# Performance work log

Measured on AMD Instinct MI355X. Metric: run time of the kernel, lower is better.

The kernel has to match this reference:

```python
import jax, jax.numpy as jnp
import numpy as np

N = 50000          # nodes
E = 1600000        # edges (before self-loops)
IN = 512           # in_channels
H = 8              # heads
C1 = 8             # per-head channels of conv1 (== heads)
OUT = 64           # out_channels
SLOPE = 0.2        # GATConv leaky_relu negative slope


def setup_inputs() -> dict:
    key = jax.random.key(0)
    ks = jax.random.split(key, 10)
    x = jax.random.normal(ks[0], (N, IN), jnp.float32)
    edge_index = jax.random.randint(ks[1], (2, E), 0, N, dtype=jnp.int64)
    s1 = 1.0 / np.sqrt(IN)
    s2 = 1.0 / np.sqrt(H * C1)
    W1 = jax.random.normal(ks[2], (IN, H * C1), jnp.float32) * s1
    att_src1 = jax.random.normal(ks[3], (H, C1), jnp.float32) * s2
    att_dst1 = jax.random.normal(ks[4], (H, C1), jnp.float32) * s2
    b1 = jnp.zeros((H * C1,), jnp.float32)
    W2 = jax.random.normal(ks[5], (H * C1, OUT), jnp.float32) * s2
    att_src2 = jax.random.normal(ks[6], (1, OUT), jnp.float32) * 0.1
    att_dst2 = jax.random.normal(ks[7], (1, OUT), jnp.float32) * 0.1
    b2 = jnp.zeros((OUT,), jnp.float32)
    return {"x": x, "edge_index": edge_index, "W1": W1, "att_src1": att_src1,
            "att_dst1": att_dst1, "b1": b1, "W2": W2, "att_src2": att_src2,
            "att_dst2": att_dst2, "b2": b2}


def gat_layer(x, src, dst, W, a_src, a_dst, b, heads, ch, concat):
    n = x.shape[0]
    h = (x @ W).reshape(n, heads, ch)                       # [N,H,C]
    alpha_src = jnp.einsum('nhc,hc->nh', h, a_src)          # [N,H]
    alpha_dst = jnp.einsum('nhc,hc->nh', h, a_dst)
    e = jax.nn.leaky_relu(alpha_src[src] + alpha_dst[dst], SLOPE)  # [Etot,H]
    # segment softmax over incoming edges of each destination node
    m = jax.ops.segment_max(e, dst, num_segments=n)
    ex = jnp.exp(e - m[dst])
    denom = jax.ops.segment_sum(ex, dst, num_segments=n)
    alpha = ex / (denom[dst] + 1e-16)                       # [Etot,H]
    out = jax.ops.segment_sum(h[src] * alpha[:, :, None], dst, num_segments=n)
    out = out.reshape(n, heads * ch) if concat else out.mean(axis=1)
    return out + b


def reference(x, edge_index, W1, att_src1, att_dst1, b1, W2, att_src2, att_dst2, b2):
    n = x.shape[0]
    loops = jnp.arange(n, dtype=edge_index.dtype)           # add_self_loops=True
    src = jnp.concatenate([edge_index[0], loops])
    dst = jnp.concatenate([edge_index[1], loops])
    h = jax.nn.elu(gat_layer(x, src, dst, W1, att_src1, att_dst1, b1, H, C1, True))
    # F.dropout in eval mode is identity
    out = gat_layer(h, src, dst, W2, att_src2, att_dst2, b2, 1, OUT, False)
    return jax.nn.log_softmax(out, axis=-1)
```

## Files before the change

kernel.cpp:

```cpp
#include <hip/hip_runtime.h>
#include <hip/hip_bf16.h>
#include <math.h>


#define WAVE 64
#define NPB_SHIFT 7
#define NB_MAX 512
#define NBLK 128
#define CAP 6144

__device__ inline float wred_sum(float v) {
#pragma unroll
    for (int off = 32; off > 0; off >>= 1) v += __shfl_xor(v, off);
    return v;
}
__device__ inline float wred_max(float v) {
#pragma unroll
    for (int off = 32; off > 0; off >>= 1) v = fmaxf(v, __shfl_xor(v, off));
    return v;
}

__global__ __launch_bounds__(256) void bucket_count(const int* __restrict__ ei,
                                                    int* __restrict__ hist,
                                                    int E, int Et, int NB, int epb) {
    __shared__ int lh[NB_MAX];
    for (int t = threadIdx.x; t < NB; t += 256) lh[t] = 0;
    __syncthreads();
    int e0 = blockIdx.x * epb;
    int e1 = min(e0 + epb, Et);
    for (int e = e0 + threadIdx.x; e < e1; e += 256) {
        int d = (e < E) ? ei[E + e] : (e - E);
        atomicAdd(&lh[d >> NPB_SHIFT], 1);
    }
    __syncthreads();
    for (int t = threadIdx.x; t < NB; t += 256)
        hist[blockIdx.x * NB + t] = lh[t];
}

__global__ __launch_bounds__(512) void bucket_scan(int* __restrict__ hist,
                                                   int* __restrict__ bBase,
                                                   int* __restrict__ rowptr,
                                                   int NB, int nblk, int n) {
    __shared__ int tot[NB_MAX];
    for (int b = threadIdx.x; b < NB; b += 512) {
        int s = 0;
        for (int j = 0; j < nblk; ++j) s += hist[j * NB + b];
        tot[b] = s;
    }
    __syncthreads();
    if (threadIdx.x == 0) {
        int run = 0;
        for (int b = 0; b < NB; ++b) { int t = tot[b]; tot[b] = run; bBase[b] = run; run += t; }
        bBase[NB] = run;
        rowptr[n] = run;
    }
    __syncthreads();
    for (int b = threadIdx.x; b < NB; b += 512) {
        int run = tot[b];
        for (int j = 0; j < nblk; ++j) { int t = hist[j * NB + b]; hist[j * NB + b] = run; run += t; }
    }
}

__global__ __launch_bounds__(256) void bucket_scatter(const int* __restrict__ ei,
                                                      const int* __restrict__ hist,
                                                      unsigned* __restrict__ region,
                                                      int E, int Et, int NB, int epb) {
    __shared__ int gb[NB_MAX];
    __shared__ int off[NB_MAX];
    for (int t = threadIdx.x; t < NB; t += 256) { gb[t] = hist[blockIdx.x * NB + t]; off[t] = 0; }
    __syncthreads();
    int e0 = blockIdx.x * epb;
    int e1 = min(e0 + epb, Et);
    for (int e = e0 + threadIdx.x; e < e1; e += 256) {
        int s, d;
        if (e < E) { s = ei[e]; d = ei[E + e]; }
        else       { s = d = e - E; }
        int b = d >> NPB_SHIFT;
        int p = gb[b] + atomicAdd(&off[b], 1);
        region[p] = (unsigned)s | ((unsigned)(d & 127) << 16);
    }
}

__global__ __launch_bounds__(256) void bucket_build(unsigned* __restrict__ region,
                                                    const int* __restrict__ bBase,
                                                    int* __restrict__ rowptr, int n) {
    __shared__ int deg[128], rp[129], cur[128];
    __shared__ unsigned short sb[CAP];
    int b = blockIdx.x;
    int base = bBase[b];
    int cnt  = min(bBase[b + 1] - base, CAP);
    int tid  = threadIdx.x;
    if (tid < 128) { deg[tid] = 0; cur[tid] = 0; }
    __syncthreads();
    for (int i = tid; i < cnt; i += 256)
        atomicAdd(&deg[region[base + i] >> 16], 1);
    __syncthreads();
    if (tid == 0) {
        int run = 0;
        for (int t = 0; t < 128; ++t) { rp[t] = run; run += deg[t]; }
        rp[128] = run;
    }
    __syncthreads();
    int nodeLo = b << NPB_SHIFT;
    if (tid < 128 && nodeLo + tid < n) rowptr[nodeLo + tid] = base + rp[tid];
    for (int i = tid; i < cnt; i += 256) {
        unsigned v = region[base + i];
        int dl = v >> 16;
        int p = rp[dl] + atomicAdd(&cur[dl], 1);
        sb[p] = (unsigned short)(v & 0xFFFFu);
    }
    __syncthreads();
    for (int i = tid; i < cnt; i += 256)
        region[base + i] = (unsigned)sb[i];
}

__global__ __launch_bounds__(256) void gemm64(const float* __restrict__ X,
                                              const float* __restrict__ W,
                                              float* __restrict__ O, int nrows, int K) {
    __shared__ float xs[32][68];
    __shared__ float ws[32][68];
    int tid = threadIdx.x;
    int bm = blockIdx.x * 64;
    int tx = tid & 15;
    int ty = tid >> 4;
    float acc[4][4] = {{0.f}};
    for (int k0 = 0; k0 < K; k0 += 32) {
#pragma unroll
        for (int i = 0; i < 2; ++i) {
            int p = tid + i * 256;
            int row = p >> 3, k4 = p & 7;
            float4 v = {0.f, 0.f, 0.f, 0.f};
            if (bm + row < nrows)
                v = *(const float4*)(X + (size_t)(bm + row) * K + k0 + k4 * 4);
            xs[k4 * 4 + 0][row] = v.x; xs[k4 * 4 + 1][row] = v.y;
            xs[k4 * 4 + 2][row] = v.z; xs[k4 * 4 + 3][row] = v.w;
        }
#pragma unroll
        for (int i = 0; i < 2; ++i) {
            int p = tid + i * 256;
            int kr = p >> 4, c4 = p & 15;
            float4 v = *(const float4*)(W + (size_t)(k0 + kr) * 64 + c4 * 4);
            ws[kr][c4 * 4 + 0] = v.x; ws[kr][c4 * 4 + 1] = v.y;
            ws[kr][c4 * 4 + 2] = v.z; ws[kr][c4 * 4 + 3] = v.w;
        }
        __syncthreads();
#pragma unroll
        for (int kk = 0; kk < 32; ++kk) {
            float a[4], bq[4];
#pragma unroll
            for (int i = 0; i < 4; ++i) a[i] = xs[kk][ty * 4 + i];
#pragma unroll
            for (int j = 0; j < 4; ++j) bq[j] = ws[kk][tx * 4 + j];
#pragma unroll
            for (int i = 0; i < 4; ++i)
#pragma unroll
                for (int j = 0; j < 4; ++j) acc[i][j] = fmaf(a[i], bq[j], acc[i][j]);
        }
        __syncthreads();
    }
    int row0 = bm + ty * 4;
#pragma unroll
    for (int i = 0; i < 4; ++i) {
        int r = row0 + i;
        if (r < nrows) {
            float4 v = {acc[i][0], acc[i][1], acc[i][2], acc[i][3]};
            *(float4*)(O + (size_t)r * 64 + tx * 4) = v;
        }
    }
}

__global__ __launch_bounds__(256) void alpha1_kernel(const float* __restrict__ H1,
                                                     const float* __restrict__ as1,
                                                     const float* __restrict__ ad1,
                                                     float* __restrict__ asrc,
                                                     float* __restrict__ adst, int n) {
    int idx = blockIdx.x * 256 + threadIdx.x;
    if (idx >= n * 8) return;
    int h = idx & 7;
    const float* hp = H1 + (size_t)(idx >> 3) * 64 + h * 8;
    float s = 0.f, d = 0.f;
#pragma unroll
    for (int c = 0; c < 8; ++c) {
        float v = hp[c];
        s = fmaf(v, as1[h * 8 + c], s);
        d = fmaf(v, ad1[h * 8 + c], d);
    }
    asrc[idx] = s;
    adst[idx] = d;
}

__global__ __launch_bounds__(256) void alpha2_kernel(const float* __restrict__ H2,
                                                     const float* __restrict__ as2,
                                                     const float* __restrict__ ad2,
                                                     float* __restrict__ asrc,
                                                     float* __restrict__ adst, int n) {
    int node = blockIdx.x * 4 + (threadIdx.x >> 6);
    int lane = threadIdx.x & 63;
    if (node >= n) return;
    float v = H2[(size_t)node * 64 + lane];
    float s = wred_sum(v * as2[lane]);
    float d = wred_sum(v * ad2[lane]);
    if (lane == 0) { asrc[node] = s; adst[node] = d; }
}

__global__ __launch_bounds__(256) void agg1_kernel(const float* __restrict__ H1,
                                                   const float* __restrict__ asrc,
                                                   const float* __restrict__ adst,
                                                   const int* __restrict__ rowptr,
                                                   const int* __restrict__ csrc,
                                                   const float* __restrict__ b1,
                                                   float* __restrict__ out1, int n) {
    __shared__ float wbuf[4][64][8];
    __shared__ int   sbuf[4][64];
    int wid  = threadIdx.x >> 6;
    int lane = threadIdx.x & 63;
    int node = blockIdx.x * 4 + wid;
    if (node >= n) return;
    int h = lane >> 3;
    int beg = rowptr[node], end = rowptr[node + 1];

    float ad[8];
    *(float4*)&ad[0] = *(const float4*)&adst[(size_t)node * 8];
    *(float4*)&ad[4] = *(const float4*)&adst[(size_t)node * 8 + 4];

    float lsum[8];
#pragma unroll
    for (int i = 0; i < 8; ++i) lsum[i] = 0.f;
    float acc0 = 0.f, acc1 = 0.f;

    for (int c0 = beg; c0 < end; c0 += 64) {
        int e = c0 + lane;
        if (e < end) {
            int s = csrc[e];
            sbuf[wid][lane] = s;
            float a[8], p[8];
            *(float4*)&a[0] = *(const float4*)&asrc[(size_t)s * 8];
            *(float4*)&a[4] = *(const float4*)&asrc[(size_t)s * 8 + 4];
#pragma unroll
            for (int i = 0; i < 8; ++i) {
                float t = a[i] + ad[i];
                t = t > 0.f ? t : 0.2f * t;
                p[i] = __expf(t);
                lsum[i] += p[i];
            }
            *(float4*)&wbuf[wid][lane][0] = *(float4*)&p[0];
            *(float4*)&wbuf[wid][lane][4] = *(float4*)&p[4];
        }
        int cnt = min(64, end - c0);
        int i = 0;
        for (; i + 3 < cnt; i += 4) {
            int s0 = sbuf[wid][i + 0], s1 = sbuf[wid][i + 1];
            int s2 = sbuf[wid][i + 2], s3 = sbuf[wid][i + 3];
            float w0 = wbuf[wid][i + 0][h], w1 = wbuf[wid][i + 1][h];
            float w2 = wbuf[wid][i + 2][h], w3 = wbuf[wid][i + 3][h];
            float g0 = H1[(size_t)s0 * 64 + lane];
            float g1 = H1[(size_t)s1 * 64 + lane];
            float g2 = H1[(size_t)s2 * 64 + lane];
            float g3 = H1[(size_t)s3 * 64 + lane];
            acc0 = fmaf(g0, w0, acc0);
            acc1 = fmaf(g1, w1, acc1);
            acc0 = fmaf(g2, w2, acc0);
            acc1 = fmaf(g3, w3, acc1);
        }
        for (; i < cnt; ++i) {
            int s   = sbuf[wid][i];
            float w = wbuf[wid][i][h];
            acc0 = fmaf(H1[(size_t)s * 64 + lane], w, acc0);
        }
    }
    float acc = acc0 + acc1;
#pragma unroll
    for (int off = 32; off > 0; off >>= 1)
#pragma unroll
        for (int i = 0; i < 8; ++i) lsum[i] += __shfl_xor(lsum[i], off);
    float L = lsum[0];
#pragma unroll
    for (int i = 1; i < 8; ++i) if (h == i) L = lsum[i];
    float o = acc / (L + 1e-16f) + b1[lane];
    out1[(size_t)node * 64 + lane] = o > 0.f ? o : expm1f(o);
}

__global__ __launch_bounds__(256) void agg2_kernel(const float* __restrict__ H2,
                                                   const float* __restrict__ asrc,
                                                   const float* __restrict__ adst,
                                                   const int* __restrict__ rowptr,
                                                   const int* __restrict__ csrc,
                                                   const float* __restrict__ b2,
                                                   float* __restrict__ out, int n) {
    __shared__ float wbuf[4][64];
    __shared__ int   sbuf[4][64];
    int wid  = threadIdx.x >> 6;
    int lane = threadIdx.x & 63;
    int node = blockIdx.x * 4 + wid;
    if (node >= n) return;
    int beg = rowptr[node], end = rowptr[node + 1];
    float ad = adst[node];

    float lsum = 0.f, acc0 = 0.f, acc1 = 0.f;
    for (int c0 = beg; c0 < end; c0 += 64) {
        int e = c0 + lane;
        if (e < end) {
            int s = csrc[e];
            sbuf[wid][lane] = s;
            float t = asrc[s] + ad;
            t = t > 0.f ? t : 0.2f * t;
            float p = __expf(t);
            lsum += p;
            wbuf[wid][lane] = p;
        }
        int cnt = min(64, end - c0);
        int i = 0;
        for (; i + 3 < cnt; i += 4) {
            int s0 = sbuf[wid][i + 0], s1 = sbuf[wid][i + 1];
            int s2 = sbuf[wid][i + 2], s3 = sbuf[wid][i + 3];
            float w0 = wbuf[wid][i + 0], w1 = wbuf[wid][i + 1];
            float w2 = wbuf[wid][i + 2], w3 = wbuf[wid][i + 3];
            float g0 = H2[(size_t)s0 * 64 + lane];
            float g1 = H2[(size_t)s1 * 64 + lane];
            float g2 = H2[(size_t)s2 * 64 + lane];
            float g3 = H2[(size_t)s3 * 64 + lane];
            acc0 = fmaf(g0, w0, acc0);
            acc1 = fmaf(g1, w1, acc1);
            acc0 = fmaf(g2, w2, acc0);
            acc1 = fmaf(g3, w3, acc1);
        }
        for (; i < cnt; ++i) {
            acc0 = fmaf(H2[(size_t)sbuf[wid][i] * 64 + lane], wbuf[wid][i], acc0);
        }
    }
    lsum = wred_sum(lsum);
    float o = (acc0 + acc1) / (lsum + 1e-16f) + b2[lane];
    float mx = wred_max(o);
    float se = wred_sum(__expf(o - mx));
    out[(size_t)node * 64 + lane] = o - mx - logf(se);
}

extern "C" void kernel_launch(void* const* d_in, const int* in_sizes, int n_in,
                              void* d_out, int out_size, void* d_ws, size_t ws_size,
                              hipStream_t stream) {
    const float* x   = (const float*)d_in[0];
    const int*   ei  = (const int*)d_in[1];
    const float* W1  = (const float*)d_in[2];
    const float* as1 = (const float*)d_in[3];
    const float* ad1 = (const float*)d_in[4];
    const float* b1  = (const float*)d_in[5];
    const float* W2  = (const float*)d_in[6];
    const float* as2 = (const float*)d_in[7];
    const float* ad2 = (const float*)d_in[8];
    const float* b2  = (const float*)d_in[9];
    float* out = (float*)d_out;

    const int n  = in_sizes[0] / 512;
    const int E  = in_sizes[1] / 2;
    const int Et = E + n;
    const int NB  = (n + 127) >> NPB_SHIFT;
    const int epb = (Et + NBLK - 1) / NBLK;

    char* w = (char*)d_ws;
    auto alloc = [&](size_t bytes) {
        char* p = w;
        w += (bytes + 255) & ~(size_t)255;
        return p;
    };
    int*      hist   = (int*)alloc((size_t)NBLK * NB * 4);
    int*      bBase  = (int*)alloc((size_t)(NB + 1) * 4);
    unsigned* region = (unsigned*)alloc((size_t)Et * 4);
    int*      rowptr = (int*)alloc((size_t)(n + 1) * 4);
    float*    h1     = (float*)alloc((size_t)n * 64 * 4);
    float*    out1   = (float*)alloc((size_t)n * 64 * 4);
    float*    h2     = (float*)alloc((size_t)n * 64 * 4);
    float*    asrc1  = (float*)alloc((size_t)n * 8 * 4);
    float*    adst1  = (float*)alloc((size_t)n * 8 * 4);
    float*    asrc2  = (float*)alloc((size_t)n * 4);
    float*    adst2  = (float*)alloc((size_t)n * 4);
    int*      csrc   = (int*)region;

    bucket_count  <<<NBLK, 256, 0, stream>>>(ei, hist, E, Et, NB, epb);
    bucket_scan   <<<1,    512, 0, stream>>>(hist, bBase, rowptr, NB, NBLK, n);
    bucket_scatter<<<NBLK, 256, 0, stream>>>(ei, hist, region, E, Et, NB, epb);
    bucket_build  <<<NB,   256, 0, stream>>>(region, bBase, rowptr, n);

    gemm64<<<(n + 63) / 64, 256, 0, stream>>>(x, W1, h1, n, 512);
    alpha1_kernel<<<(n * 8 + 255) / 256, 256, 0, stream>>>(h1, as1, ad1, asrc1, adst1, n);
    agg1_kernel<<<(n + 3) / 4, 256, 0, stream>>>(h1, asrc1, adst1, rowptr, csrc, b1, out1, n);

    gemm64<<<(n + 63) / 64, 256, 0, stream>>>(out1, W2, h2, n, 64);
    alpha2_kernel<<<(n + 3) / 4, 256, 0, stream>>>(h2, as2, ad2, asrc2, adst2, n);
    agg2_kernel<<<(n + 3) / 4, 256, 0, stream>>>(h2, asrc2, adst2, rowptr, csrc, b2, out, n);
}
```

Before: 460.1 us.

## Replace first-layer FP32 GEMM with bf16 MFMA kernel

Result: faster. 440.5 us (-4.3%).

```diff
diff --git a/kernel.cpp b/kernel.cpp
--- a/kernel.cpp
+++ b/kernel.cpp
@@ -9,6 +9,9 @@
 #define NBLK 128
 #define CAP 6144
 
+typedef __attribute__((ext_vector_type(8))) short short8;
+typedef __attribute__((ext_vector_type(4))) float f32x4;
+
 __device__ inline float wred_sum(float v) {
 #pragma unroll
     for (int off = 32; off > 0; off >>= 1) v += __shfl_xor(v, off);
@@ -18,6 +21,11 @@
 #pragma unroll
     for (int off = 32; off > 0; off >>= 1) v = fmaxf(v, __shfl_xor(v, off));
     return v;
+}
+__device__ inline unsigned short f2bf(float f) {
+    unsigned u = __float_as_uint(f);
+    u += 0x7FFFu + ((u >> 16) & 1u);
+    return (unsigned short)(u >> 16);
 }
 
 __global__ __launch_bounds__(256) void bucket_count(const int* __restrict__ ei,
@@ -112,6 +120,63 @@
     __syncthreads();
     for (int i = tid; i < cnt; i += 256)
         region[base + i] = (unsigned)sb[i];
+}
+
+__global__ __launch_bounds__(256) void wtrans_kernel(const float* __restrict__ W,
+                                                     unsigned short* __restrict__ wtg) {
+    int idx = blockIdx.x * 256 + threadIdx.x;
+    if (idx >= 64 * 512) return;
+    int c = idx >> 9, k = idx & 511;
+    wtg[c * 512 + k] = f2bf(W[k * 64 + c]);
+}
+
+__global__ __launch_bounds__(256) void gemm1_mfma(const float* __restrict__ X,
+                                                  const unsigned short* __restrict__ wtg,
+                                                  float* __restrict__ O, int nrows) {
+    __shared__ unsigned short xs[64][40];
+    __shared__ unsigned short wt[64][40];
+    int tid  = threadIdx.x;
+    int wid  = tid >> 6;
+    int lane = tid & 63;
+    int lr   = lane & 15;
+    int lg   = lane >> 4;
+    int bm   = blockIdx.x * 64;
+
+    f32x4 acc[4];
+#pragma unroll
+    for (int i = 0; i < 4; ++i) acc[i] = (f32x4){0.f, 0.f, 0.f, 0.f};
+
+    for (int k0 = 0; k0 < 512; k0 += 32) {
+#pragma unroll
+        for (int i = 0; i < 2; ++i) {
+            int p = tid + i * 256;
+            int row = p >> 3, c4 = p & 7;
+            float4 v = {0.f, 0.f, 0.f, 0.f};
+            if (bm + row < nrows)
+                v = *(const float4*)(X + (size_t)(bm + row) * 512 + k0 + c4 * 4);
+            unsigned short* dst = &xs[row][c4 * 4];
+            dst[0] = f2bf(v.x); dst[1] = f2bf(v.y); dst[2] = f2bf(v.z); dst[3] = f2bf(v.w);
+        }
+        {
+            int c = tid >> 2, kq = tid & 3;
+            *(short8*)&wt[c][kq * 8] = *(const short8*)&wtg[c * 512 + k0 + kq * 8];
+        }
+        __syncthreads();
+        short8 af = *(short8*)&xs[wid * 16 + lr][lg * 8];
+#pragma unroll
+        for (int cb = 0; cb < 4; ++cb) {
+            short8 bfb = *(short8*)&wt[cb * 16 + lr][lg * 8];
+            acc[cb] = __builtin_amdgcn_mfma_f32_16x16x32_bf16(af, bfb, acc[cb], 0, 0, 0);
+        }
+        __syncthreads();
+    }
+#pragma unroll
+    for (int cb = 0; cb < 4; ++cb)
+#pragma unroll
+        for (int r = 0; r < 4; ++r) {
+            int m = bm + wid * 16 + lg * 4 + r;
+            if (m < nrows) O[(size_t)m * 64 + cb * 16 + lr] = acc[cb][r];
+        }
 }
 
 __global__ __launch_bounds__(256) void gemm64(const float* __restrict__ X,
@@ -362,25 +427,27 @@
         w += (bytes + 255) & ~(size_t)255;
         return p;
     };
-    int*      hist   = (int*)alloc((size_t)NBLK * NB * 4);
-    int*      bBase  = (int*)alloc((size_t)(NB + 1) * 4);
-    unsigned* region = (unsigned*)alloc((size_t)Et * 4);
-    int*      rowptr = (int*)alloc((size_t)(n + 1) * 4);
-    float*    h1     = (float*)alloc((size_t)n * 64 * 4);
-    float*    out1   = (float*)alloc((size_t)n * 64 * 4);
-    float*    h2     = (float*)alloc((size_t)n * 64 * 4);
-    float*    asrc1  = (float*)alloc((size_t)n * 8 * 4);
-    float*    adst1  = (float*)alloc((size_t)n * 8 * 4);
-    float*    asrc2  = (float*)alloc((size_t)n * 4);
-    float*    adst2  = (float*)alloc((size_t)n * 4);
-    int*      csrc   = (int*)region;
+    int*            hist   = (int*)alloc((size_t)NBLK * NB * 4);
+    int*            bBase  = (int*)alloc((size_t)(NB + 1) * 4);
+    unsigned*       region = (unsigned*)alloc((size_t)Et * 4);
+    int*            rowptr = (int*)alloc((size_t)(n + 1) * 4);
+    float*          h1     = (float*)alloc((size_t)n * 64 * 4);
+    float*          out1   = (float*)alloc((size_t)n * 64 * 4);
+    float*          h2     = (float*)alloc((size_t)n * 64 * 4);
+    float*          asrc1  = (float*)alloc((size_t)n * 8 * 4);
+    float*          adst1  = (float*)alloc((size_t)n * 8 * 4);
+    float*          asrc2  = (float*)alloc((size_t)n * 4);
+    float*          adst2  = (float*)alloc((size_t)n * 4);
+    unsigned short* wtg    = (unsigned short*)alloc((size_t)64 * 512 * 2);
+    int*            csrc   = (int*)region;
 
     bucket_count  <<<NBLK, 256, 0, stream>>>(ei, hist, E, Et, NB, epb);
     bucket_scan   <<<1,    512, 0, stream>>>(hist, bBase, rowptr, NB, NBLK, n);
     bucket_scatter<<<NBLK, 256, 0, stream>>>(ei, hist, region, E, Et, NB, epb);
     bucket_build  <<<NB,   256, 0, stream>>>(region, bBase, rowptr, n);
 
-    gemm64<<<(n + 63) / 64, 256, 0, stream>>>(x, W1, h1, n, 512);
+    wtrans_kernel<<<(64 * 512 + 255) / 256, 256, 0, stream>>>(W1, wtg);
+    gemm1_mfma<<<(n + 63) / 64, 256, 0, stream>>>(x, wtg, h1, n);
     alpha1_kernel<<<(n * 8 + 255) / 256, 256, 0, stream>>>(h1, as1, ad1, asrc1, adst1, n);
     agg1_kernel<<<(n + 3) / 4, 256, 0, stream>>>(h1, asrc1, adst1, rowptr, csrc, b1, out1, n);
 
```
